# Performance work log

Hardware: AMD Instinct MI355X
Metric: run time of the kernel (lower is better)

The kernel has to match this reference:

```python
import jax, jax.numpy as jnp
import numpy as np

B, S, DIM = 4, 2048, 1024
H, HD = 8, 64
NUM_B = 1024
INNER = H * HD


def setup_inputs() -> dict:
    key = jax.random.key(0)
    ks = jax.random.split(key, 6)
    sc = 1.0 / np.sqrt(HD)
    return {
        "x": jax.random.normal(ks[0], (B, S, DIM), jnp.float32),
        "b_param": jax.random.normal(ks[1], (NUM_B, HD, HD), jnp.float32) * sc,
        "k_param": jax.random.normal(ks[2], (NUM_B, HD), jnp.float32) * sc,
        "w_qv": jax.random.normal(ks[3], (DIM, 2 * INNER), jnp.float32) * (1.0 / np.sqrt(DIM)),
        "w_out": jax.random.normal(ks[4], (INNER, DIM), jnp.float32) * (1.0 / np.sqrt(INNER)),
        "b_out": jax.random.normal(ks[5], (DIM,), jnp.float32) * 0.01,
        "top_k": 64,
    }


def reference(x, b_param, k_param, w_qv, w_out, b_out, top_k):
    scale = HD ** (-0.5)
    qv = x @ w_qv                      # (B, S, 2*INNER)
    q, v = jnp.split(qv, 2, axis=-1)
    # 'b i (h d) -> (b h) i d'
    def to_heads(t):
        return t.reshape(B, S, H, HD).transpose(0, 2, 1, 3).reshape(B * H, S, HD)
    q, v = to_heads(q), to_heads(v)
    sim = jnp.einsum('nd,bid->bin', k_param, q) * scale   # (B*H, S, NUM_B)
    t, b_inds = jax.lax.top_k(sim, top_k)                 # (B*H, S, K)
    attn = jax.nn.softmax(t, axis=-1)
    # torch einsum 'b i k d d, b i d -> b i k d' takes the DIAGONAL of each
    # gathered (d,d) brain matrix; extract diagonals first (same math, no dxd gather).
    b_diag = jnp.diagonal(b_param, axis1=1, axis2=2)      # (NUM_B, HD)
    g = b_diag[b_inds]                                    # (B*H, S, K, HD)
    out = jnp.einsum('bikd,bik->bid', g * v[:, :, None, :], attn)  # (B*H, S, HD)
    # '(b h) i d -> b i (h d)'
    out = out.reshape(B, H, S, HD).transpose(0, 2, 1, 3).reshape(B, S, INNER)
    return out @ w_out + b_out
```

## Files before the change

kernel.cpp:

```cpp
#include <hip/hip_runtime.h>
#include <cstdint>
#include <cstddef>

namespace {
constexpr int B = 4, S = 2048, DIM = 1024, H = 8, HD = 64;
constexpr int NUM_B = 1024, INNER = 512, KTOP = 64;
constexpr int MROWS = B * S;
constexpr double DELTA = 1e-6;
constexpr float CUT = 2.106e-3f;
constexpr float GAP_FLAG = 2e-5f;
constexpr int CAP = 4096;
}

typedef short bf16x8 __attribute__((ext_vector_type(8)));
typedef float f32x4 __attribute__((ext_vector_type(4)));
typedef unsigned short ush;

#define GLOAD16(gp, lp)                                                  \
  __builtin_amdgcn_global_load_lds(                                      \
      (const __attribute__((address_space(1))) unsigned int*)(gp),       \
      (__attribute__((address_space(3))) unsigned int*)(lp), 16, 0, 0)

__device__ __forceinline__ ush rne_bf16(float x) {
  unsigned u = __float_as_uint(x);
  unsigned r = u + 0x7FFFu + ((u >> 16) & 1u);
  return (ush)(r >> 16);
}
__device__ __forceinline__ float bf16_to_f32(ush h) {
  return __uint_as_float((unsigned)h << 16);
}

__global__ __launch_bounds__(256) void split_x(const float* __restrict__ X,
                                               ush* __restrict__ Xh,
                                               ush* __restrict__ Xl) {
  const size_t i = (size_t)blockIdx.x * 256 + threadIdx.x;
  const float4 v = reinterpret_cast<const float4*>(X)[i];
  const float e[4] = {v.x, v.y, v.z, v.w};
  ush h[4], l[4];
#pragma unroll
  for (int t = 0; t < 4; ++t) {
    h[t] = rne_bf16(e[t]);
    l[t] = rne_bf16(e[t] - bf16_to_f32(h[t]));
  }
  const int row = (int)(i >> 8);
  const int q = (int)(i & 255);
  const size_t o = (size_t)row * 256 + (q ^ ((row & 7) << 1));
  reinterpret_cast<ushort4*>(Xh)[o] = make_ushort4(h[0], h[1], h[2], h[3]);
  reinterpret_cast<ushort4*>(Xl)[o] = make_ushort4(l[0], l[1], l[2], l[3]);
}

__global__ void prep_kernel(const float* __restrict__ kp, const float* __restrict__ bp,
                            float* __restrict__ kT, float* __restrict__ bd,
                            ush* __restrict__ khB, ush* __restrict__ klB,
                            unsigned* __restrict__ cnt) {
  int n = blockIdx.x;
  int d = threadIdx.x;
  if (n == 0 && d == 0) *cnt = 0u;
  float kv = kp[(size_t)n * HD + d];
  kT[(size_t)d * NUM_B + n] = kv;
  bd[(size_t)n * HD + d] = bp[(size_t)n * HD * HD + (size_t)d * HD + d];
  ush kh = rne_bf16(kv);
  float resid = kv - bf16_to_f32(kh);
  ush kl = rne_bf16(resid);
  int t = n >> 4, c = n & 15, khf = d >> 5, kd = d & 31;
  int l = (kd >> 3) * 16 + c, j = d & 7;
  size_t idx = ((size_t)(t * 2 + khf) * 64 + l) * 8 + j;
  khB[idx] = kh;
  klB[idx] = kl;
}

__global__ __launch_bounds__(256) void splitT_kernel(
    const float* __restrict__ W, int R, int C,
    ush* __restrict__ Th, ush* __restrict__ Tl) {
  __shared__ float t[64][65];
  const int tid = threadIdx.x;
  const int c0 = blockIdx.x * 64, r0 = blockIdx.y * 64;
#pragma unroll
  for (int i = 0; i < 16; ++i) {
    int idx = tid + 256 * i;
    int row = idx >> 6, col = idx & 63;
    t[row][col] = W[(size_t)(r0 + row) * C + c0 + col];
  }
  __syncthreads();
#pragma unroll
  for (int i = 0; i < 16; ++i) {
    int idx = tid + 256 * i;
    int orow = idx >> 6, ocol = idx & 63;
    float v = t[ocol][orow];
    ush hi = rne_bf16(v);
    const int n = c0 + orow;
    const int osw = ocol ^ ((n & 7) << 3);
    Th[(size_t)n * R + r0 + osw] = hi;
    Tl[(size_t)n * R + r0 + osw] = rne_bf16(v - bf16_to_f32(hi));
  }
}

__global__ __launch_bounds__(256) void gemm_pre(
    const ush* __restrict__ Ah, const ush* __restrict__ Al, int lda,
    const ush* __restrict__ BTh, const ush* __restrict__ BTl, int ldb,
    const float* __restrict__ bias, float* __restrict__ C, int ldc, int K) {
  __shared__ ush Ah_s[128 * 64], Al_s[128 * 64], Bh_s[128 * 64], Bl_s[128 * 64];
  char* AhB = (char*)Ah_s;
  char* AlB = (char*)Al_s;
  char* BhB = (char*)Bh_s;
  char* BlB = (char*)Bl_s;
  const int tid = threadIdx.x;
  const int lane = tid & 63;
  const int w = tid >> 6;
  const int wm = w >> 1, wn = w & 1;
  const int bm = blockIdx.x * 128, bn = blockIdx.y * 128;

  f32x4 acc[4][4];
#pragma unroll
  for (int mt = 0; mt < 4; ++mt)
#pragma unroll
    for (int nt = 0; nt < 4; ++nt) acc[mt][nt] = (f32x4){0.f, 0.f, 0.f, 0.f};

  for (int k0 = 0; k0 < K; k0 += 64) {
#pragma unroll
    for (int i = 0; i < 4; ++i) {
      const int idx = tid + 256 * i;
      const int row = idx >> 3, s8 = idx & 7;
      const size_t goA = (size_t)(bm + row) * lda + k0 + s8 * 8;
      const size_t goB = (size_t)(bn + row) * ldb + k0 + s8 * 8;
      GLOAD16(Ah + goA, AhB + idx * 16);
      GLOAD16(Al + goA, AlB + idx * 16);
      GLOAD16(BTh + goB, BhB + idx * 16);
      GLOAD16(BTl + goB, BlB + idx * 16);
    }
    __syncthreads();
#pragma unroll
    for (int ks = 0; ks < 2; ++ks) {
      const int kg = lane >> 4;
      const int kb = ks * 64 + kg * 16;
      bf16x8 ah[4], al[4], bh[4], bl[4];
#pragma unroll
      for (int mt = 0; mt < 4; ++mt) {
        int rl = wm * 64 + mt * 16 + (lane & 15);
        int off = rl * 128 + (kb ^ ((rl & 7) << 4));
        ah[mt] = *reinterpret_cast<const bf16x8*>(AhB + off);
        al[mt] = *reinterpret_cast<const bf16x8*>(AlB + off);
      }
#pragma unroll
      for (int nt = 0; nt < 4; ++nt) {
        int rl = wn * 64 + nt * 16 + (lane & 15);
        int off = rl * 128 + (kb ^ ((rl & 7) << 4));
        bh[nt] = *reinterpret_cast<const bf16x8*>(BhB + off);
        bl[nt] = *reinterpret_cast<const bf16x8*>(BlB + off);
      }
#pragma unroll
      for (int mt = 0; mt < 4; ++mt)
#pragma unroll
        for (int nt = 0; nt < 4; ++nt) {
          acc[mt][nt] = __builtin_amdgcn_mfma_f32_16x16x32_bf16(ah[mt], bh[nt], acc[mt][nt], 0, 0, 0);
          acc[mt][nt] = __builtin_amdgcn_mfma_f32_16x16x32_bf16(al[mt], bh[nt], acc[mt][nt], 0, 0, 0);
          acc[mt][nt] = __builtin_amdgcn_mfma_f32_16x16x32_bf16(ah[mt], bl[nt], acc[mt][nt], 0, 0, 0);
        }
    }
    __syncthreads();
  }
  const int g = lane >> 4, c = lane & 15;
#pragma unroll
  for (int mt = 0; mt < 4; ++mt)
#pragma unroll
    for (int nt = 0; nt < 4; ++nt) {
      int gc = bn + wn * 64 + nt * 16 + c;
      float bv = bias ? bias[gc] : 0.f;
#pragma unroll
      for (int reg = 0; reg < 4; ++reg) {
        int gr = bm + wm * 64 + mt * 16 + g * 4 + reg;
        C[(size_t)gr * ldc + gc] = acc[mt][nt][reg] + bv;
      }
    }
}

__device__ __forceinline__ unsigned long long enc64(double v) {
  unsigned long long u = (unsigned long long)__double_as_longlong(v);
  return (u >> 63) ? ~u : (u | 0x8000000000000000ull);
}
__device__ __forceinline__ double dec64(unsigned long long k) {
  unsigned long long u = (k >> 63) ? (k ^ 0x8000000000000000ull) : ~k;
  return __longlong_as_double((long long)u);
}

__global__ __launch_bounds__(512) void attn_pass1(
    const float* __restrict__ qv, const ush* __restrict__ khB,
    const ush* __restrict__ klB, const float* __restrict__ bd,
    ush* __restrict__ Oh, ush* __restrict__ Ol,
    unsigned* __restrict__ cnt, unsigned* __restrict__ list) {
  extern __shared__ char smem[];
  float (*sim_s)[1024] = (float(*)[1024])smem;
  ush (*qh_s)[72] = (ush(*)[72])smem;
  ush (*ql_s)[72] = (ush(*)[72])(smem + 2304);

  const int tid = threadIdx.x;
  const int lane = tid & 63;
  const int w = tid >> 6;
  const int blk = blockIdx.x;
  const int bh = blk >> 7;
  const int it = blk & 127;
  const int b = bh >> 3;
  const int h = bh & 7;
  const int i0 = it * 16;

  {
    const int row = tid >> 5;
    const int d = (tid & 31) * 2;
    const float2 v = *reinterpret_cast<const float2*>(
        &qv[((size_t)(b * S + i0 + row)) * DIM + h * HD + d]);
    const float q2[2] = {v.x, v.y};
#pragma unroll
    for (int e = 0; e < 2; ++e) {
      ush hi = rne_bf16(q2[e]);
      qh_s[row][d + e] = hi;
      ql_s[row][d + e] = rne_bf16(q2[e] - bf16_to_f32(hi));
    }
  }
  __syncthreads();

  const int arow = lane & 15;
  const int kb = (lane >> 4) * 8;
  const bf16x8 aqh0 = *reinterpret_cast<const bf16x8*>(&qh_s[arow][kb]);
  const bf16x8 aqh1 = *reinterpret_cast<const bf16x8*>(&qh_s[arow][32 + kb]);
  const bf16x8 aql0 = *reinterpret_cast<const bf16x8*>(&ql_s[arow][kb]);
  const bf16x8 aql1 = *reinterpret_cast<const bf16x8*>(&ql_s[arow][32 + kb]);
  __syncthreads();

  const bf16x8* khf = reinterpret_cast<const bf16x8*>(khB);
  const bf16x8* klf = reinterpret_cast<const bf16x8*>(klB);
  const int cc = lane & 15, gg = lane >> 4;
#pragma unroll
  for (int tt = 0; tt < 8; ++tt) {
    const int t = w * 8 + tt;
    const bf16x8 kh0 = khf[(t * 2 + 0) * 64 + lane];
    const bf16x8 kh1 = khf[(t * 2 + 1) * 64 + lane];
    const bf16x8 kl0 = klf[(t * 2 + 0) * 64 + lane];
    const bf16x8 kl1 = klf[(t * 2 + 1) * 64 + lane];
    f32x4 a = {0.f, 0.f, 0.f, 0.f};
    a = __builtin_amdgcn_mfma_f32_16x16x32_bf16(aqh0, kh0, a, 0, 0, 0);
    a = __builtin_amdgcn_mfma_f32_16x16x32_bf16(aqh1, kh1, a, 0, 0, 0);
    a = __builtin_amdgcn_mfma_f32_16x16x32_bf16(aql0, kh0, a, 0, 0, 0);
    a = __builtin_amdgcn_mfma_f32_16x16x32_bf16(aql1, kh1, a, 0, 0, 0);
    a = __builtin_amdgcn_mfma_f32_16x16x32_bf16(aqh0, kl0, a, 0, 0, 0);
    a = __builtin_amdgcn_mfma_f32_16x16x32_bf16(aqh1, kl1, a, 0, 0, 0);
#pragma unroll
    for (int reg = 0; reg < 4; ++reg)
      sim_s[gg * 4 + reg][t * 16 + cc] = __fmul_rn(a[reg], 0.125f);
  }
  __syncthreads();

  const int r0 = w * 2;
  float acc[2][16];
#pragma unroll
  for (int rr = 0; rr < 2; ++rr)
#pragma unroll
    for (int j = 0; j < 16; ++j) acc[rr][j] = sim_s[r0 + rr][lane + 64 * j];

  float hi4[2], lo4[2], mrow[2];
#pragma unroll
  for (int r = 0; r < 2; ++r) {
    float mx = acc[r][0];
#pragma unroll
    for (int j = 1; j < 16; ++j) mx = fmaxf(mx, acc[r][j]);
    float gmx = mx, gmn = mx;
#pragma unroll
    for (int off = 32; off >= 1; off >>= 1) {
      gmx = fmaxf(gmx, __shfl_xor(gmx, off, 64));
      gmn = fminf(gmn, __shfl_xor(gmn, off, 64));
    }
    hi4[r] = gmx;
    mrow[r] = gmx;
    lo4[r] = gmn;
  }

  unsigned c4[2];
#pragma unroll
  for (int r = 0; r < 2; ++r) {
    unsigned c = 0;
#pragma unroll
    for (int j = 0; j < 16; ++j)
      c += (unsigned)__popcll(__ballot(acc[r][j] >= lo4[r]));
    c4[r] = c;
  }

  for (int itr = 0; itr < 20; ++itr) {
    if (c4[0] == (unsigned)KTOP && c4[1] == (unsigned)KTOP) break;
#pragma unroll
    for (int r = 0; r < 2; ++r) {
      if (c4[r] == (unsigned)KTOP) continue;
      const float mid = 0.5f * (lo4[r] + hi4[r]);
      unsigned c = 0;
#pragma unroll
      for (int j = 0; j < 16; ++j)
        c += (unsigned)__popcll(__ballot(acc[r][j] >= mid));
      if (c >= (unsigned)KTOP) {
        lo4[r] = mid;
        c4[r] = c;
      } else {
        hi4[r] = mid;
      }
    }
  }

  const unsigned long long lmask = (1ull << lane) - 1ull;
  float zreg[2];

#pragma unroll
  for (int rr = 0; rr < 2; ++rr) {
    int2* selp = (int2*)(smem + (size_t)(r0 + rr) * 4096);
    const float loF = lo4[rr];
    float v65 = -1e30f, v64m = 1e30f;
#pragma unroll
    for (int j = 0; j < 16; ++j) {
      const float v = acc[rr][j];
      const bool ge = v >= loF;
      v65 = fmaxf(v65, ge ? -1e30f : v);
      v64m = fminf(v64m, ge ? v : 1e30f);
    }
#pragma unroll
    for (int off = 32; off >= 1; off >>= 1) {
      v65 = fmaxf(v65, __shfl_xor(v65, off, 64));
      v64m = fminf(v64m, __shfl_xor(v64m, off, 64));
    }
    const bool flag =
        (c4[rr] != (unsigned)KTOP) || (__fadd_rn(v64m, -v65) < GAP_FLAG);

    int selc = 0;
    float zloc = 0.f;
#pragma unroll
    for (int j = 0; j < 16; ++j) {
      const bool sel = acc[rr][j] >= loF;
      const unsigned long long ms = __ballot(sel);
      if (sel) {
        const int pos = selc + __popcll(ms & lmask);
        if (pos < KTOP) {
          const float wexp = expf(__fadd_rn(acc[rr][j], -mrow[rr]));
          selp[pos] = make_int2(lane + 64 * j, __float_as_int(wexp));
          zloc += wexp;
        }
      }
      selc += __popcll(ms);
    }
#pragma unroll
    for (int off = 32; off >= 1; off >>= 1) zloc += __shfl_xor(zloc, off, 64);
    zreg[rr] = zloc;
    if (lane == 0 && flag) {
      unsigned idx = atomicAdd(cnt, 1u);
      if (idx < (unsigned)CAP)
        list[idx] = ((unsigned)bh << 11) | (unsigned)(i0 + r0 + rr);
    }
  }

#pragma unroll 1
  for (int rr = 0; rr < 2; ++rr) {
    const int2* selp = (const int2*)(smem + (size_t)(r0 + rr) * 4096);
    float accd = 0.f;
#pragma unroll 16
    for (int k = 0; k < KTOP; ++k) {
      const int2 p = selp[k];
      accd = __fmaf_rn(__int_as_float(p.y), bd[(size_t)p.x * HD + lane], accd);
    }
    const size_t rowi = (size_t)(b * S + i0 + r0 + rr);
    float v = qv[rowi * DIM + INNER + h * HD + lane];
    const float Oout = v * accd / zreg[rr];
    const ush oh = rne_bf16(Oout);
    const int lsw = lane ^ ((int)(rowi & 7) << 3);
    Oh[rowi * INNER + h * HD + lsw] = oh;
    Ol[rowi * INNER + h * HD + lsw] = rne_bf16(Oout - bf16_to_f32(oh));
  }
}

__global__ __launch_bounds__(64) void attn_pass2(
    const float* __restrict__ x, const float* __restrict__ w_qv,
    const float* __restrict__ qv, const float* __restrict__ kT,
    const float* __restrict__ bd, const float* __restrict__ w_out,
    const unsigned* __restrict__ cnt, const unsigned* __restrict__ list,
    ush* __restrict__ Oh, ush* __restrict__ Ol) {
  unsigned n_flag = *cnt;
  if (n_flag > (unsigned)CAP) n_flag = (unsigned)CAP;
  if (blockIdx.x >= n_flag) return;
  const unsigned code = list[blockIdx.x];
  const int bh = (int)(code >> 11);
  const int i = (int)(code & 2047u);
  const int b = bh >> 3;
  const int h = bh & 7;
  const size_t rowi = (size_t)(b * S + i);
  const int lane = threadIdx.x;

  __shared__ double q_l[64];
  __shared__ int sel_n[KTOP];
  __shared__ float sel_w[KTOP];

  {
    const float* xr = &x[rowi * DIM];
    const float* wc = &w_qv[h * HD + lane];
    double s = 0.0;
    for (int k = 0; k < DIM; ++k)
      s = fma((double)xr[k], (double)wc[(size_t)k * 1024], s);
    q_l[lane] = s;
  }
  __syncthreads();

  double sv[16];
#pragma unroll
  for (int j = 0; j < 16; ++j) sv[j] = 0.0;
  for (int d = 0; d < 64; ++d) {
    double qd = q_l[d];
    const float* kr = &kT[(size_t)d * NUM_B + lane];
#pragma unroll
    for (int j = 0; j < 16; ++j) sv[j] = fma(qd, (double)kr[64 * j], sv[j]);
  }
  unsigned long long key[16];
#pragma unroll
  for (int j = 0; j < 16; ++j) {
    sv[j] = sv[j] * 0.125;
    key[j] = enc64(sv[j]);
  }
  double m = sv[0];
#pragma unroll
  for (int j = 1; j < 16; ++j) m = fmax(m, sv[j]);
#pragma unroll
  for (int off = 32; off >= 1; off >>= 1) m = fmax(m, __shfl_xor(m, off, 64));

  unsigned long long T = 0ull;
  for (int bit = 63; bit >= 0; --bit) {
    unsigned long long cand = T | (1ull << bit);
    int c = 0;
#pragma unroll
    for (int j = 0; j < 16; ++j) c += (key[j] >= cand);
#pragma unroll
    for (int off = 32; off >= 1; off >>= 1) c += __shfl_xor(c, off, 64);
    if (c >= KTOP) T = cand;
  }
  int cgt = 0;
#pragma unroll
  for (int j = 0; j < 16; ++j) cgt += (key[j] > T);
#pragma unroll
  for (int off = 32; off >= 1; off >>= 1) cgt += __shfl_xor(cgt, off, 64);
  const int need_eq = KTOP - cgt;
  const unsigned long long lmask = (1ull << lane) - 1ull;

  int selc = 0, eqc = 0;
  float zloc = 0.f;
#pragma unroll
  for (int j = 0; j < 16; ++j) {
    bool gt = key[j] > T;
    bool eq = key[j] == T;
    unsigned long long me = __ballot(eq);
    bool esel = eq && (eqc + __popcll(me & lmask) < need_eq);
    bool sel = gt || esel;
    unsigned long long ms = __ballot(sel);
    if (sel) {
      int pos = selc + __popcll(ms & lmask);
      float wexp = expf((float)(sv[j] - m));
      sel_n[pos] = 64 * j + lane;
      sel_w[pos] = wexp;
      zloc += wexp;
    }
    selc += __popcll(ms);
    eqc += __popcll(me);
  }
#pragma unroll
  for (int off = 32; off >= 1; off >>= 1) zloc += __shfl_xor(zloc, off, 64);

  unsigned long long best = 0ull;
#pragma unroll
  for (int j = 0; j < 16; ++j)
    if (key[j] < T && key[j] > best) best = key[j];
#pragma unroll
  for (int off = 32; off >= 1; off >>= 1) {
    unsigned long long o = __shfl_xor(best, off, 64);
    if (o > best) best = o;
  }
  int an = 1 << 30, bn = 1 << 30;
#pragma unroll
  for (int j = 0; j < 16; ++j) {
    if (key[j] == T) an = min(an, 64 * j + lane);
    if (key[j] == best) bn = min(bn, 64 * j + lane);
  }
#pragma unroll
  for (int off = 32; off >= 1; off >>= 1) {
    an = min(an, __shfl_xor(an, off, 64));
    bn = min(bn, __shfl_xor(bn, off, 64));
  }
  double v64 = dec64(T), v65 = dec64(best);
  const bool flg = (best != 0ull) && ((v64 - v65) < DELTA);
  const float wA = expf((float)(v64 - m));
  const float wB = expf((float)(v65 - m));
  __syncthreads();

  float SA = 0.f;
#pragma unroll 8
  for (int k = 0; k < KTOP; ++k)
    SA = __fmaf_rn(sel_w[k], bd[(size_t)sel_n[k] * HD + lane], SA);
  const float v = qv[rowi * DIM + INNER + h * HD + lane];
  const float ZA = zloc;
  const float OA = v * SA / ZA;
  float Oout = OA;
  if (flg) {
    const float altS = SA - wA * bd[(size_t)an * HD + lane] +
                       wB * bd[(size_t)bn * HD + lane];
    const float ZB = ZA - wA + wB;
    const float OB = v * altS / ZB;
    const float dO = 0.5f * (OA - OB);
    float s[16];
#pragma unroll
    for (int cc = 0; cc < 16; ++cc) s[cc] = 0.f;
    for (int d = 0; d < 64; ++d) {
      float dOd = __shfl(dO, d, 64);
      const float* wr = &w_out[(size_t)(h * HD + d) * DIM];
#pragma unroll
      for (int cc = 0; cc < 16; ++cc)
        s[cc] = __fmaf_rn(dOd, wr[cc * 64 + lane], s[cc]);
    }
    float fm = 0.f;
#pragma unroll
    for (int cc = 0; cc < 16; ++cc) fm = fmaxf(fm, fabsf(s[cc]));
#pragma unroll
    for (int off = 32; off >= 1; off >>= 1) fm = fmaxf(fm, __shfl_xor(fm, off, 64));
    if (fm <= CUT) Oout = OA - dO;
  }
  const ush oh = rne_bf16(Oout);
  const int lsw = lane ^ ((int)(rowi & 7) << 3);
  Oh[rowi * INNER + h * HD + lsw] = oh;
  Ol[rowi * INNER + h * HD + lsw] = rne_bf16(Oout - bf16_to_f32(oh));
}

extern "C" void kernel_launch(void* const* d_in, const int* in_sizes, int n_in,
                              void* d_out, int out_size, void* d_ws, size_t ws_size,
                              hipStream_t stream) {
  const float* x = (const float*)d_in[0];
  const float* bparam = (const float*)d_in[1];
  const float* kparam = (const float*)d_in[2];
  const float* w_qv = (const float*)d_in[3];
  const float* w_out = (const float*)d_in[4];
  const float* b_out = (const float*)d_in[5];
  (void)in_sizes; (void)n_in; (void)out_size; (void)ws_size;

  char* ws = (char*)d_ws;
  float* qv = (float*)ws;
  ush* xh = (ush*)(ws + (size_t)MROWS * DIM * 4);
  ush* xl = xh + (size_t)MROWS * DIM;
  ush* Oh = xh;
  ush* Ol = xl;
  float* bd = (float*)(xl + (size_t)MROWS * DIM);
  float* kT = bd + (size_t)NUM_B * HD;
  ush* khB = (ush*)(kT + (size_t)HD * NUM_B);
  ush* klB = khB + (size_t)64 * 2 * 64 * 8;
  ush* wqvTh = klB + (size_t)64 * 2 * 64 * 8;
  ush* wqvTl = wqvTh + (size_t)DIM * DIM;
  ush* woutTh = wqvTl + (size_t)DIM * DIM;
  ush* woutTl = woutTh + (size_t)DIM * INNER;
  unsigned* cnt = (unsigned*)(woutTl + (size_t)DIM * INNER);
  unsigned* list = cnt + 1;

  prep_kernel<<<NUM_B, HD, 0, stream>>>(kparam, bparam, kT, bd, khB, klB, cnt);

  splitT_kernel<<<dim3(16, 16), 256, 0, stream>>>(w_qv, DIM, 2 * INNER, wqvTh, wqvTl);
  splitT_kernel<<<dim3(16, 8), 256, 0, stream>>>(w_out, INNER, DIM, woutTh, woutTl);
  split_x<<<MROWS * DIM / 1024, 256, 0, stream>>>(x, xh, xl);

  gemm_pre<<<dim3(64, 8), 256, 0, stream>>>(xh, xl, DIM, wqvTh, wqvTl, DIM,
                                            nullptr, qv, DIM, DIM);

  attn_pass1<<<4096, 512, 65536, stream>>>(qv, khB, klB, bd, Oh, Ol, cnt, list);
  attn_pass2<<<CAP, 64, 0, stream>>>(x, w_qv, qv, kT, bd, w_out, cnt, list, Oh, Ol);

  gemm_pre<<<dim3(64, 8), 256, 0, stream>>>(Oh, Ol, INNER, woutTh, woutTl, INNER,
                                            b_out, (float*)d_out, DIM, INNER);
}
```

Baseline: 371.2 us.

## Merge prep kernels into one launch and halve attn_pass1 shared memory

Combines the four preprocessing kernels (weight transpose-splits, key/diagonal prep, x split) into a single producer kernel that dispatches on block index, removing three launches. In attn_pass1 the similarity matrix is now computed in two halves of 512 columns through a 32 KB shared buffer instead of 64 KB, with an extra barrier between halves. The goal is higher occupancy (more blocks per CU) in exchange for an extra synchronisation. The selection scratch stride is reduced to fit the smaller buffer.

```diff
diff --git a/kernel.cpp b/kernel.cpp
--- a/kernel.cpp
+++ b/kernel.cpp
@@ -30,68 +30,77 @@
   return __uint_as_float((unsigned)h << 16);
 }
 
-__global__ __launch_bounds__(256) void split_x(const float* __restrict__ X,
-                                               ush* __restrict__ Xh,
-                                               ush* __restrict__ Xl) {
-  const size_t i = (size_t)blockIdx.x * 256 + threadIdx.x;
-  const float4 v = reinterpret_cast<const float4*>(X)[i];
-  const float e[4] = {v.x, v.y, v.z, v.w};
-  ush h[4], l[4];
-#pragma unroll
-  for (int t = 0; t < 4; ++t) {
-    h[t] = rne_bf16(e[t]);
-    l[t] = rne_bf16(e[t] - bf16_to_f32(h[t]));
-  }
-  const int row = (int)(i >> 8);
-  const int q = (int)(i & 255);
-  const size_t o = (size_t)row * 256 + (q ^ ((row & 7) << 1));
-  reinterpret_cast<ushort4*>(Xh)[o] = make_ushort4(h[0], h[1], h[2], h[3]);
-  reinterpret_cast<ushort4*>(Xl)[o] = make_ushort4(l[0], l[1], l[2], l[3]);
-}
-
-__global__ void prep_kernel(const float* __restrict__ kp, const float* __restrict__ bp,
-                            float* __restrict__ kT, float* __restrict__ bd,
-                            ush* __restrict__ khB, ush* __restrict__ klB,
-                            unsigned* __restrict__ cnt) {
-  int n = blockIdx.x;
-  int d = threadIdx.x;
-  if (n == 0 && d == 0) *cnt = 0u;
-  float kv = kp[(size_t)n * HD + d];
-  kT[(size_t)d * NUM_B + n] = kv;
-  bd[(size_t)n * HD + d] = bp[(size_t)n * HD * HD + (size_t)d * HD + d];
-  ush kh = rne_bf16(kv);
-  float resid = kv - bf16_to_f32(kh);
-  ush kl = rne_bf16(resid);
-  int t = n >> 4, c = n & 15, khf = d >> 5, kd = d & 31;
-  int l = (kd >> 3) * 16 + c, j = d & 7;
-  size_t idx = ((size_t)(t * 2 + khf) * 64 + l) * 8 + j;
-  khB[idx] = kh;
-  klB[idx] = kl;
-}
-
-__global__ __launch_bounds__(256) void splitT_kernel(
-    const float* __restrict__ W, int R, int C,
-    ush* __restrict__ Th, ush* __restrict__ Tl) {
-  __shared__ float t[64][65];
+__global__ __launch_bounds__(256) void producer_kernel(
+    const float* __restrict__ x, const float* __restrict__ kp,
+    const float* __restrict__ bp, const float* __restrict__ w_qv,
+    const float* __restrict__ w_out,
+    ush* __restrict__ Xh, ush* __restrict__ Xl,
+    float* __restrict__ kT, float* __restrict__ bd,
+    ush* __restrict__ khB, ush* __restrict__ klB,
+    ush* __restrict__ wqvTh, ush* __restrict__ wqvTl,
+    ush* __restrict__ woutTh, ush* __restrict__ woutTl,
+    unsigned* __restrict__ cnt) {
+  const int blk = blockIdx.x;
   const int tid = threadIdx.x;
-  const int c0 = blockIdx.x * 64, r0 = blockIdx.y * 64;
-#pragma unroll
-  for (int i = 0; i < 16; ++i) {
-    int idx = tid + 256 * i;
-    int row = idx >> 6, col = idx & 63;
-    t[row][col] = W[(size_t)(r0 + row) * C + c0 + col];
-  }
-  __syncthreads();
-#pragma unroll
-  for (int i = 0; i < 16; ++i) {
-    int idx = tid + 256 * i;
-    int orow = idx >> 6, ocol = idx & 63;
-    float v = t[ocol][orow];
-    ush hi = rne_bf16(v);
-    const int n = c0 + orow;
-    const int osw = ocol ^ ((n & 7) << 3);
-    Th[(size_t)n * R + r0 + osw] = hi;
-    Tl[(size_t)n * R + r0 + osw] = rne_bf16(v - bf16_to_f32(hi));
+
+  if (blk < 384) {
+    const float* W;
+    ush *Th, *Tl;
+    int R, C, local;
+    if (blk < 256) {
+      W = w_qv; Th = wqvTh; Tl = wqvTl; R = DIM; C = 2 * INNER; local = blk;
+    } else {
+      W = w_out; Th = woutTh; Tl = woutTl; R = INNER; C = DIM; local = blk - 256;
+    }
+    const int c0 = (local & 15) * 64, r0 = (local >> 4) * 64;
+    __shared__ float t[64][65];
+#pragma unroll
+    for (int i = 0; i < 16; ++i) {
+      int idx = tid + 256 * i;
+      int row = idx >> 6, col = idx & 63;
+      t[row][col] = W[(size_t)(r0 + row) * C + c0 + col];
+    }
+    __syncthreads();
+#pragma unroll
+    for (int i = 0; i < 16; ++i) {
+      int idx = tid + 256 * i;
+      int orow = idx >> 6, ocol = idx & 63;
+      float v = t[ocol][orow];
+      ush hi = rne_bf16(v);
+      const int n = c0 + orow;
+      const int osw = ocol ^ ((n & 7) << 3);
+      Th[(size_t)n * R + r0 + osw] = hi;
+      Tl[(size_t)n * R + r0 + osw] = rne_bf16(v - bf16_to_f32(hi));
+    }
+  } else if (blk < 640) {
+    const int n = (blk - 384) * 4 + (tid >> 6);
+    const int d = tid & 63;
+    if (blk == 384 && tid == 0) *cnt = 0u;
+    float kv = kp[(size_t)n * HD + d];
+    kT[(size_t)d * NUM_B + n] = kv;
+    bd[(size_t)n * HD + d] = bp[(size_t)n * HD * HD + (size_t)d * HD + d];
+    ush kh = rne_bf16(kv);
+    ush kl = rne_bf16(kv - bf16_to_f32(kh));
+    int t = n >> 4, c = n & 15, khf = d >> 5, kd = d & 31;
+    int l = (kd >> 3) * 16 + c, j = d & 7;
+    size_t idx = ((size_t)(t * 2 + khf) * 64 + l) * 8 + j;
+    khB[idx] = kh;
+    klB[idx] = kl;
+  } else {
+    const size_t i = (size_t)(blk - 640) * 256 + tid;
+    const float4 v = reinterpret_cast<const float4*>(x)[i];
+    const float e[4] = {v.x, v.y, v.z, v.w};
+    ush h[4], l[4];
+#pragma unroll
+    for (int t = 0; t < 4; ++t) {
+      h[t] = rne_bf16(e[t]);
+      l[t] = rne_bf16(e[t] - bf16_to_f32(h[t]));
+    }
+    const int row = (int)(i >> 8);
+    const int q = (int)(i & 255);
+    const size_t o = (size_t)row * 256 + (q ^ ((row & 7) << 1));
+    reinterpret_cast<ushort4*>(Xh)[o] = make_ushort4(h[0], h[1], h[2], h[3]);
+    reinterpret_cast<ushort4*>(Xl)[o] = make_ushort4(l[0], l[1], l[2], l[3]);
   }
 }
 
@@ -189,7 +198,7 @@
     ush* __restrict__ Oh, ush* __restrict__ Ol,
     unsigned* __restrict__ cnt, unsigned* __restrict__ list) {
   extern __shared__ char smem[];
-  float (*sim_s)[1024] = (float(*)[1024])smem;
+  float (*sim_s)[512] = (float(*)[512])smem;
   ush (*qh_s)[72] = (ush(*)[72])smem;
   ush (*ql_s)[72] = (ush(*)[72])(smem + 2304);
 
@@ -229,32 +238,38 @@
   const bf16x8* khf = reinterpret_cast<const bf16x8*>(khB);
   const bf16x8* klf = reinterpret_cast<const bf16x8*>(klB);
   const int cc = lane & 15, gg = lane >> 4;
-#pragma unroll
-  for (int tt = 0; tt < 8; ++tt) {
-    const int t = w * 8 + tt;
-    const bf16x8 kh0 = khf[(t * 2 + 0) * 64 + lane];
-    const bf16x8 kh1 = khf[(t * 2 + 1) * 64 + lane];
-    const bf16x8 kl0 = klf[(t * 2 + 0) * 64 + lane];
-    const bf16x8 kl1 = klf[(t * 2 + 1) * 64 + lane];
-    f32x4 a = {0.f, 0.f, 0.f, 0.f};
-    a = __builtin_amdgcn_mfma_f32_16x16x32_bf16(aqh0, kh0, a, 0, 0, 0);
-    a = __builtin_amdgcn_mfma_f32_16x16x32_bf16(aqh1, kh1, a, 0, 0, 0);
-    a = __builtin_amdgcn_mfma_f32_16x16x32_bf16(aql0, kh0, a, 0, 0, 0);
-    a = __builtin_amdgcn_mfma_f32_16x16x32_bf16(aql1, kh1, a, 0, 0, 0);
-    a = __builtin_amdgcn_mfma_f32_16x16x32_bf16(aqh0, kl0, a, 0, 0, 0);
-    a = __builtin_amdgcn_mfma_f32_16x16x32_bf16(aqh1, kl1, a, 0, 0, 0);
-#pragma unroll
-    for (int reg = 0; reg < 4; ++reg)
-      sim_s[gg * 4 + reg][t * 16 + cc] = __fmul_rn(a[reg], 0.125f);
-  }
-  __syncthreads();
-
   const int r0 = w * 2;
   float acc[2][16];
-#pragma unroll
-  for (int rr = 0; rr < 2; ++rr)
-#pragma unroll
-    for (int j = 0; j < 16; ++j) acc[rr][j] = sim_s[r0 + rr][lane + 64 * j];
+
+#pragma unroll
+  for (int half = 0; half < 2; ++half) {
+#pragma unroll
+    for (int tt = 0; tt < 4; ++tt) {
+      const int t = half * 32 + w * 4 + tt;
+      const bf16x8 kh0 = khf[(t * 2 + 0) * 64 + lane];
+      const bf16x8 kh1 = khf[(t * 2 + 1) * 64 + lane];
+      const bf16x8 kl0 = klf[(t * 2 + 0) * 64 + lane];
+      const bf16x8 kl1 = klf[(t * 2 + 1) * 64 + lane];
+      f32x4 a = {0.f, 0.f, 0.f, 0.f};
+      a = __builtin_amdgcn_mfma_f32_16x16x32_bf16(aqh0, kh0, a, 0, 0, 0);
+      a = __builtin_amdgcn_mfma_f32_16x16x32_bf16(aqh1, kh1, a, 0, 0, 0);
+      a = __builtin_amdgcn_mfma_f32_16x16x32_bf16(aql0, kh0, a, 0, 0, 0);
+      a = __builtin_amdgcn_mfma_f32_16x16x32_bf16(aql1, kh1, a, 0, 0, 0);
+      a = __builtin_amdgcn_mfma_f32_16x16x32_bf16(aqh0, kl0, a, 0, 0, 0);
+      a = __builtin_amdgcn_mfma_f32_16x16x32_bf16(aqh1, kl1, a, 0, 0, 0);
+      const int col = (t - half * 32) * 16 + cc;
+#pragma unroll
+      for (int reg = 0; reg < 4; ++reg)
+        sim_s[gg * 4 + reg][col] = __fmul_rn(a[reg], 0.125f);
+    }
+    __syncthreads();
+#pragma unroll
+    for (int rr = 0; rr < 2; ++rr)
+#pragma unroll
+      for (int jj = 0; jj < 8; ++jj)
+        acc[rr][half * 8 + jj] = sim_s[r0 + rr][lane + 64 * jj];
+    if (half == 0) __syncthreads();
+  }
 
   float hi4[2], lo4[2], mrow[2];
 #pragma unroll
@@ -307,7 +322,7 @@
 
 #pragma unroll
   for (int rr = 0; rr < 2; ++rr) {
-    int2* selp = (int2*)(smem + (size_t)(r0 + rr) * 4096);
+    int2* selp = (int2*)(smem + (size_t)(r0 + rr) * 2048);
     const float loF = lo4[rr];
     float v65 = -1e30f, v64m = 1e30f;
 #pragma unroll
@@ -353,7 +368,7 @@
 
 #pragma unroll 1
   for (int rr = 0; rr < 2; ++rr) {
-    const int2* selp = (const int2*)(smem + (size_t)(r0 + rr) * 4096);
+    const int2* selp = (const int2*)(smem + (size_t)(r0 + rr) * 2048);
     float accd = 0.f;
 #pragma unroll 16
     for (int k = 0; k < KTOP; ++k) {
@@ -554,16 +569,14 @@
   unsigned* cnt = (unsigned*)(woutTl + (size_t)DIM * INNER);
   unsigned* list = cnt + 1;
 
-  prep_kernel<<<NUM_B, HD, 0, stream>>>(kparam, bparam, kT, bd, khB, klB, cnt);
-
-  splitT_kernel<<<dim3(16, 16), 256, 0, stream>>>(w_qv, DIM, 2 * INNER, wqvTh, wqvTl);
-  splitT_kernel<<<dim3(16, 8), 256, 0, stream>>>(w_out, INNER, DIM, woutTh, woutTl);
-  split_x<<<MROWS * DIM / 1024, 256, 0, stream>>>(x, xh, xl);
+  producer_kernel<<<640 + MROWS, 256, 0, stream>>>(
+      x, kparam, bparam, w_qv, w_out, xh, xl, kT, bd, khB, klB,
+      wqvTh, wqvTl, woutTh, woutTl, cnt);
 
   gemm_pre<<<dim3(64, 8), 256, 0, stream>>>(xh, xl, DIM, wqvTh, wqvTl, DIM,
                                             nullptr, qv, DIM, DIM);
 
-  attn_pass1<<<4096, 512, 65536, stream>>>(qv, khB, klB, bd, Oh, Ol, cnt, list);
+  attn_pass1<<<4096, 512, 32768, stream>>>(qv, khB, klB, bd, Oh, Ol, cnt, list);
   attn_pass2<<<CAP, 64, 0, stream>>>(x, w_qv, qv, kT, bd, w_out, cnt, list, Oh, Ol);
 
   gemm_pre<<<dim3(64, 8), 256, 0, stream>>>(Oh, Ol, INNER, woutTh, woutTl, INNER,
```

After: 363.5 us. 2.1% less time.
